# Kernel optimization log

Hardware: AMD Instinct MI355X
Metric: run time of the kernel (lower is better)

Reference implementation:

```python
import jax, jax.numpy as jnp
import numpy as np

N_E, FEAT, REST = 2048, 512, 8
HEAD, LENGTH = 8, 64


def setup_inputs() -> dict:
    key = jax.random.key(0)
    kx, kq, kk, kd = jax.random.split(key, 4)
    x = jax.random.normal(kx, (N_E, FEAT, REST), dtype=jnp.float32)
    Q = jax.random.normal(kq, (HEAD, LENGTH, FEAT), dtype=jnp.float32)
    K = jax.random.normal(kk, (HEAD, LENGTH, FEAT), dtype=jnp.float32)
    D = jax.random.normal(kd, (HEAD, LENGTH, FEAT), dtype=jnp.float32)
    return {"x": x, "Q": Q, "K": K, "D": D}


def _linear(a, W):
    # a: (n, f, *rest), W: (h, q, f) -> y: (n, h, q, *rest)
    y = jnp.einsum('nf...,hqf->nhq...', a, W)
    # L2-normalize over the last 3 axes (here: h? no -- axes (q, rest...) per the
    # original code: sum over (-1,-2,-3) of (n,h,q,rest) = (h,q,rest) per n)
    norm = jnp.sqrt((y * y).sum((-1, -2, -3), keepdims=True))
    return y / norm


def reference(x, Q, K, D):
    n_e = x.shape[0]
    rest = x.shape[2:]
    head, length = Q.shape[0], Q.shape[1]
    q = _linear(x, Q)  # (n, h, l, rest)
    k = _linear(x, K)
    d = _linear(x, D)
    # scores over electrons: contract (l, rest) -> (h, n, n)
    w = jax.nn.softmax(jnp.einsum('nh...,mh...->hnm', q, k), axis=-1)
    # weighted combine: (h,n,m) x (m,h,l,rest) -> (n,h,l,rest)
    v = jnp.einsum('hnm,mhl...->nhl...', w, d)
    return v.reshape((n_e, head * length) + rest)
```

## Files before the change

### kernel.cpp

```cpp
#include <hip/hip_runtime.h>
#include <math.h>

#define NE   2048
#define FEAT 512

typedef short short8 __attribute__((ext_vector_type(8)));
typedef float f32x4  __attribute__((ext_vector_type(4)));

__device__ __forceinline__ unsigned short f2bf(float f) {
    union { float f; unsigned u; } v; v.f = f;
    unsigned r = v.u + 0x7fffu + ((v.u >> 16) & 1u);
    return (unsigned short)(r >> 16);
}
__device__ __forceinline__ float bf2f(unsigned b) {
    union { unsigned u; float f; } v; v.u = b << 16;
    return v.f;
}
__device__ __forceinline__ unsigned pack2(float a, float b) {
    return (unsigned)f2bf(a) | ((unsigned)f2bf(b) << 16);
}

__device__ __forceinline__ void gld16(unsigned short* lds, const unsigned short* g) {
    __builtin_amdgcn_global_load_lds(
        (const __attribute__((address_space(1))) unsigned int*)g,
        (__attribute__((address_space(3))) unsigned int*)lds,
        16, 0, 0);
}

__device__ __forceinline__ void bar() {
    asm volatile("" ::: "memory");
    __builtin_amdgcn_s_barrier();
    asm volatile("" ::: "memory");
}
#define VMW(n) asm volatile("s_waitcnt vmcnt(" #n ")" ::: "memory")


__global__ __launch_bounds__(256) void wconv_kernel(
    const float* __restrict__ Wq, const float* __restrict__ Wk, const float* __restrict__ Wd,
    unsigned short* __restrict__ wbf)
{
    const int t = threadIdx.x;
    const float* W = (blockIdx.y == 0) ? Wq : (blockIdx.y == 1) ? Wk : Wd;
    unsigned short* o = wbf + (size_t)blockIdx.y * 262144;
    const int idx = blockIdx.x * 2048 + t * 8;
    const float4* p = (const float4*)(W + idx);
    float4 v0 = p[0], v1 = p[1];
    *(uint4*)(o + idx) = make_uint4(pack2(v0.x, v0.y), pack2(v0.z, v0.w),
                                    pack2(v1.x, v1.y), pack2(v1.z, v1.w));
}

__global__ __launch_bounds__(256) void xpose_kernel(const float* __restrict__ x,
                                                    unsigned short* __restrict__ xt)
{
    __shared__ float xs[8 * 516];
    const int t = threadIdx.x;
    const int n = blockIdx.x;
    const float4* xp = (const float4*)(x + (size_t)n * 4096);
    #pragma unroll
    for (int i = 0; i < 4; ++i) {
        int idx = t + 256 * i;
        float4 v = xp[idx];
        int f = idx >> 1, rh = (idx & 1) * 4;
        xs[(rh + 0) * 516 + f] = v.x;
        xs[(rh + 1) * 516 + f] = v.y;
        xs[(rh + 2) * 516 + f] = v.z;
        xs[(rh + 3) * 516 + f] = v.w;
    }
    __syncthreads();
    const int r = t >> 5, f0 = (t & 31) * 16;
    const float* src = &xs[r * 516 + f0];
    unsigned o[8];
    #pragma unroll
    for (int j = 0; j < 8; ++j) o[j] = pack2(src[2 * j], src[2 * j + 1]);
    unsigned short* dst = xt + (size_t)n * 4096 + r * 512 + f0;
    *(uint4*)dst       = make_uint4(o[0], o[1], o[2], o[3]);
    *(uint4*)(dst + 8) = make_uint4(o[4], o[5], o[6], o[7]);
}

__global__ __launch_bounds__(512, 1) void proj_gemm(
    const unsigned short* __restrict__ wbf, const unsigned short* __restrict__ xt,
    unsigned short* __restrict__ qb, unsigned short* __restrict__ kb, unsigned short* __restrict__ db,
    float* __restrict__ s2)
{
    __shared__ unsigned short SM[49152];
    const int t = threadIdx.x;
    int bid = blockIdx.x + 128 * (blockIdx.y + 2 * blockIdx.z);
    int swz = (bid & 7) * 96 + (bid >> 3);
    const int bx = swz & 127, rest = swz >> 7;
    const int my = rest & 1, w = rest >> 1;
    const unsigned short* W = wbf + (size_t)w * 262144;
    unsigned short* out = (w == 0) ? qb : (w == 1) ? kb : db;
    const int M0 = my * 256;
    const int N0 = bx * 128;
    const int wave = t >> 6, lane = t & 63, quad = lane >> 4, l16 = lane & 15;
    const int wr = wave >> 1, wc = wave & 1;
    const int lrow = lane >> 3;
    const int scol = ((lane & 7) ^ lrow) * 8;

    f32x4 acc[4][4];
    #pragma unroll
    for (int m = 0; m < 4; ++m)
        #pragma unroll
        for (int n = 0; n < 4; ++n) acc[m][n] = {0.f, 0.f, 0.f, 0.f};

    auto STAGE = [&](int kc, int buf) {
        unsigned short* A = SM + buf * 16384;
        unsigned short* B = SM + 32768 + buf * 8192;
        #pragma unroll
        for (int p = 0; p < 4; ++p) {
            int c = p * 8 + wave;
            gld16(A + c * 512, W + (size_t)(M0 + c * 8 + lrow) * 512 + kc * 64 + scol);
        }
        #pragma unroll
        for (int p = 0; p < 2; ++p) {
            int c = p * 8 + wave;
            gld16(B + c * 512, xt + (size_t)(N0 + c * 8 + lrow) * 512 + kc * 64 + scol);
        }
    };
    auto COMPUTE = [&](int buf) {
        const unsigned short* A = SM + buf * 16384;
        const unsigned short* B = SM + 32768 + buf * 8192;
        #pragma unroll
        for (int kk = 0; kk < 2; ++kk) {
            int so = ((kk * 4 + quad) ^ (l16 & 7)) * 8;
            short8 a[4], b[4];
            #pragma unroll
            for (int m = 0; m < 4; ++m)
                a[m] = *(const short8*)&A[(wr * 64 + m * 16 + l16) * 64 + so];
            #pragma unroll
            for (int n = 0; n < 4; ++n)
                b[n] = *(const short8*)&B[(wc * 64 + n * 16 + l16) * 64 + so];
            #pragma unroll
            for (int m = 0; m < 4; ++m)
                #pragma unroll
                for (int n = 0; n < 4; ++n)
                    acc[m][n] = __builtin_amdgcn_mfma_f32_16x16x32_bf16(a[m], b[n], acc[m][n], 0, 0, 0);
        }
    };

    STAGE(0, 0);
    STAGE(1, 1);
    for (int kc = 0; kc < 8; ++kc) {
        if (kc < 7) { VMW(6); } else { VMW(0); }
        bar();
        COMPUTE(kc & 1);
        bar();
        if (kc + 2 < 8) STAGE(kc + 2, kc & 1);
    }

    float cs[4];
    #pragma unroll
    for (int n = 0; n < 4; ++n) {
        float s = 0.f;
        #pragma unroll
        for (int m = 0; m < 4; ++m)
            #pragma unroll
            for (int reg = 0; reg < 4; ++reg)
                s += acc[m][n][reg] * acc[m][n][reg];
        cs[n] = s;
    }
    #pragma unroll
    for (int n = 0; n < 4; ++n) {
        float s = cs[n];
        s += __shfl_xor(s, 16);
        s += __shfl_xor(s, 32);
        s += __shfl_xor(s, 1);
        s += __shfl_xor(s, 2);
        s += __shfl_xor(s, 4);
        if ((lane & 7) == 0 && lane < 16) {
            int n_elec = (N0 >> 3) + wc * 8 + n * 2 + (lane >> 3);
            atomicAdd(&s2[w * NE + n_elec], s);
        }
    }

    unsigned short* T = SM;
    #pragma unroll
    for (int m = 0; m < 4; ++m)
        #pragma unroll
        for (int reg = 0; reg < 4; ++reg) {
            int row = wr * 64 + m * 16 + quad * 4 + reg;
            #pragma unroll
            for (int n = 0; n < 4; ++n)
                T[row * 136 + wc * 64 + n * 16 + l16] = f2bf(acc[m][n][reg]);
        }
    __syncthreads();
    #pragma unroll
    for (int i = 0; i < 8; ++i) {
        int c = t + 512 * i;
        int row = c & 255, cb = c >> 8;
        uint4 v = *(const uint4*)(T + row * 136 + cb * 8);
        int hl = M0 + row;
        unsigned short* dst = out + (size_t)(hl >> 6) * 1048576 + (size_t)(hl & 63) * 8
                                  + (size_t)((N0 >> 3) + cb) * 512;
        *(uint4*)dst = v;
    }
}

__global__ __launch_bounds__(256) void dtrans_kernel(
    const unsigned short* __restrict__ db, const float* __restrict__ s2d,
    unsigned short* __restrict__ dT)
{
    __shared__ float Ts[64 * 68];
    const int t = threadIdx.x;
    const int h = blockIdx.z, n0 = blockIdx.y * 64, f0 = blockIdx.x * 64;
    const int rr = t >> 3, cs = (t & 7) * 8;
    #pragma unroll
    for (int p = 0; p < 2; ++p) {
        int row = rr + p * 32;
        float sc = rsqrtf(s2d[n0 + row]);
        uint4 v = *(const uint4*)(db + ((size_t)h * NE + n0 + row) * 512 + f0 + cs);
        unsigned a[4] = {v.x, v.y, v.z, v.w};
        float* d = &Ts[row * 68 + cs];
        #pragma unroll
        for (int j = 0; j < 4; ++j) {
            d[2 * j]     = bf2f(a[j] & 0xffffu) * sc;
            d[2 * j + 1] = bf2f(a[j] >> 16) * sc;
        }
    }
    __syncthreads();
    const int f = t >> 2, ns = (t & 3) * 16;
    unsigned o[8];
    #pragma unroll
    for (int j = 0; j < 8; ++j)
        o[j] = pack2(Ts[(ns + 2 * j) * 68 + f], Ts[(ns + 2 * j + 1) * 68 + f]);
    unsigned short* dst = dT + ((size_t)h * 512 + f0 + f) * NE + n0 + ns;
    *(uint4*)dst       = make_uint4(o[0], o[1], o[2], o[3]);
    *(uint4*)(dst + 8) = make_uint4(o[4], o[5], o[6], o[7]);
}

__global__ __launch_bounds__(512, 1) void score_kernel(
    const unsigned short* __restrict__ qb, const unsigned short* __restrict__ kb,
    const float* __restrict__ s2, unsigned short* __restrict__ P,
    float* __restrict__ sums, int g)
{
    __shared__ unsigned short SM[49152];
    const int t = threadIdx.x;
    int bid = blockIdx.x + 16 * (blockIdx.y + 8 * blockIdx.z);
    int swz = (bid & 7) * 64 + (bid >> 3);
    const int bx = swz & 15, by = (swz >> 4) & 7, bz = swz >> 7;
    const int hg = bz, h = g * 4 + hg;
    const int n0 = by * 256, m0 = bx * 128;
    const int wave = t >> 6, lane = t & 63, quad = lane >> 4, l16 = lane & 15;
    const int wr = wave >> 1, wc = wave & 1;
    const int lrow = lane >> 3;
    const int scol = ((lane & 7) ^ lrow) * 8;
    const unsigned short* qh = qb + (size_t)h * NE * 512;
    const unsigned short* kh = kb + (size_t)h * NE * 512;

    f32x4 acc[4][4];
    #pragma unroll
    for (int m = 0; m < 4; ++m)
        #pragma unroll
        for (int n = 0; n < 4; ++n) acc[m][n] = {0.f, 0.f, 0.f, 0.f};

    auto STAGE = [&](int kc, int buf) {
        unsigned short* A = SM + buf * 16384;
        unsigned short* B = SM + 32768 + buf * 8192;
        #pragma unroll
        for (int p = 0; p < 4; ++p) {
            int c = p * 8 + wave;
            gld16(A + c * 512, qh + (size_t)(n0 + c * 8 + lrow) * 512 + kc * 64 + scol);
        }
        #pragma unroll
        for (int p = 0; p < 2; ++p) {
            int c = p * 8 + wave;
            gld16(B + c * 512, kh + (size_t)(m0 + c * 8 + lrow) * 512 + kc * 64 + scol);
        }
    };
    auto COMPUTE = [&](int buf) {
        const unsigned short* A = SM + buf * 16384;
        const unsigned short* B = SM + 32768 + buf * 8192;
        #pragma unroll
        for (int kk = 0; kk < 2; ++kk) {
            int so = ((kk * 4 + quad) ^ (l16 & 7)) * 8;
            short8 a[4], b[4];
            #pragma unroll
            for (int m = 0; m < 4; ++m)
                a[m] = *(const short8*)&A[(wr * 64 + m * 16 + l16) * 64 + so];
            #pragma unroll
            for (int n = 0; n < 4; ++n)
                b[n] = *(const short8*)&B[(wc * 64 + n * 16 + l16) * 64 + so];
            #pragma unroll
            for (int m = 0; m < 4; ++m)
                #pragma unroll
                for (int n = 0; n < 4; ++n)
                    acc[m][n] = __builtin_amdgcn_mfma_f32_16x16x32_bf16(a[m], b[n], acc[m][n], 0, 0, 0);
        }
    };

    STAGE(0, 0);
    STAGE(1, 1);
    for (int kc = 0; kc < 8; ++kc) {
        if (kc < 7) { VMW(6); } else { VMW(0); }
        bar();
        COMPUTE(kc & 1);
        bar();
        if (kc + 2 < 8) STAGE(kc + 2, kc & 1);
    }

    float ik[4];
    #pragma unroll
    for (int n = 0; n < 4; ++n) ik[n] = rsqrtf(s2[NE + m0 + wc * 64 + n * 16 + l16]);

    unsigned short* T = SM;
    #pragma unroll
    for (int m = 0; m < 4; ++m)
        #pragma unroll
        for (int reg = 0; reg < 4; ++reg) {
            int row = wr * 64 + m * 16 + quad * 4 + reg;
            float qs = rsqrtf(s2[n0 + row]);
            float rs = 0.f;
            #pragma unroll
            for (int n = 0; n < 4; ++n) {
                float e = __expf(acc[m][n][reg] * qs * ik[n]);
                unsigned short bx16 = f2bf(e);
                T[row * 136 + wc * 64 + n * 16 + l16] = bx16;
                rs += bf2f(bx16);
            }
            rs += __shfl_xor(rs, 1);
            rs += __shfl_xor(rs, 2);
            rs += __shfl_xor(rs, 4);
            rs += __shfl_xor(rs, 8);
            if (l16 == 0) atomicAdd(&sums[hg * NE + n0 + row], rs);
        }
    __syncthreads();
    unsigned short* Ph = P + (size_t)hg * NE * NE;
    #pragma unroll
    for (int i = 0; i < 8; ++i) {
        int c = t + 512 * i;
        int row = c >> 4, cb = c & 15;
        uint4 v = *(const uint4*)(T + row * 136 + cb * 8);
        *(uint4*)(Ph + (size_t)(n0 + row) * NE + m0 + cb * 8) = v;
    }
}

__global__ __launch_bounds__(512, 1) void combine_kernel(
    const unsigned short* __restrict__ P, const unsigned short* __restrict__ dT,
    const float* __restrict__ sums, float* __restrict__ out, int g)
{
    __shared__ unsigned short Ps[2][16384];
    __shared__ unsigned short Ds[2][16384];
    const int t = threadIdx.x;
    int bid = blockIdx.x + 4 * (blockIdx.y + 16 * blockIdx.z);
    int swz = (bid & 7) * 32 + (bid >> 3);
    const int bx = swz & 3, by = (swz >> 2) & 15, bz = swz >> 6;
    const int hg = bz, h = g * 4 + hg;
    const int n0 = by * 128, f0 = bx * 128;
    const int wave = t >> 6, lane = t & 63, quad = lane >> 4, l16 = lane & 15;
    const int wn = wave >> 1, wf = wave & 1;
    const int lrow4 = lane >> 4;
    const unsigned short* Ph = P + (size_t)hg * NE * NE;
    const unsigned short* dh = dT + (size_t)h * 512 * NE;

    f32x4 acc[2][4];
    #pragma unroll
    for (int i = 0; i < 2; ++i)
        #pragma unroll
        for (int j = 0; j < 4; ++j) acc[i][j] = {0.f, 0.f, 0.f, 0.f};

    auto STAGE = [&](int mc, int buf) {
        #pragma unroll
        for (int p = 0; p < 4; ++p) {
            int c = p * 8 + wave;
            int row = c * 4 + lrow4;
            int sb = ((lane & 15) ^ (row & 15)) * 8;
            gld16(&Ps[buf][c * 512], Ph + (size_t)(n0 + row) * NE + mc * 128 + sb);
        }
        #pragma unroll
        for (int p = 0; p < 4; ++p) {
            int c = p * 8 + wave;
            int row = c * 4 + lrow4;
            int sb = ((lane & 15) ^ (row & 15)) * 8;
            gld16(&Ds[buf][c * 512], dh + (size_t)(f0 + row) * NE + mc * 128 + sb);
        }
    };
    auto COMPUTE = [&](int buf) {
        #pragma unroll
        for (int kk = 0; kk < 4; ++kk) {
            int so = ((kk * 4 + quad) ^ l16) * 8;
            short8 a0 = *(const short8*)&Ps[buf][(wn * 32 + l16) * 128 + so];
            short8 a1 = *(const short8*)&Ps[buf][(wn * 32 + 16 + l16) * 128 + so];
            #pragma unroll
            for (int ct = 0; ct < 4; ++ct) {
                short8 bb = *(const short8*)&Ds[buf][(wf * 64 + ct * 16 + l16) * 128 + so];
                acc[0][ct] = __builtin_amdgcn_mfma_f32_16x16x32_bf16(a0, bb, acc[0][ct], 0, 0, 0);
                acc[1][ct] = __builtin_amdgcn_mfma_f32_16x16x32_bf16(a1, bb, acc[1][ct], 0, 0, 0);
            }
        }
    };

    STAGE(0, 0);
    STAGE(1, 1);
    for (int mc = 0; mc < 16; ++mc) {
        if (mc < 15) { VMW(8); } else { VMW(0); }
        bar();
        COMPUTE(mc & 1);
        bar();
        if (mc + 2 < 16) STAGE(mc + 2, mc & 1);
    }

    #pragma unroll
    for (int rt = 0; rt < 2; ++rt)
        #pragma unroll
        for (int reg = 0; reg < 4; ++reg) {
            int nl = wn * 32 + rt * 16 + quad * 4 + reg;
            float li = 1.0f / sums[hg * NE + n0 + nl];
            float* orow = out + (size_t)(n0 + nl) * 4096 + h * 512 + f0 + wf * 64;
            #pragma unroll
            for (int ct = 0; ct < 4; ++ct)
                orow[ct * 16 + l16] = acc[rt][ct][reg] * li;
        }
}

extern "C" void kernel_launch(void* const* d_in, const int* in_sizes, int n_in,
                              void* d_out, int out_size, void* d_ws, size_t ws_size,
                              hipStream_t stream)
{
    const float* x  = (const float*)d_in[0];
    const float* Qw = (const float*)d_in[1];
    const float* Kw = (const float*)d_in[2];
    const float* Dw = (const float*)d_in[3];
    float* out = (float*)d_out;

    char* ws = (char*)d_ws;
    unsigned short* xt = (unsigned short*)ws;
    unsigned short* db = (unsigned short*)(ws + 16777216);
    unsigned short* P  = (unsigned short*)ws;
    unsigned short* qb = (unsigned short*)(ws + 33554432);
    unsigned short* kb = (unsigned short*)(ws + 33554432 + 16777216);
    unsigned short* dT = (unsigned short*)(ws + 33554432 + 2 * 16777216);
    unsigned short* wbf = dT;
    float* sums   = (float*)(ws + 83886080);
    float* s2     = (float*)(ws + 83886080 + 32768);

    wconv_kernel<<<dim3(128, 3), 256, 0, stream>>>(Qw, Kw, Dw, wbf);
    xpose_kernel<<<2048, 256, 0, stream>>>(x, xt);
    hipMemsetAsync(s2, 0, 3 * NE * sizeof(float), stream);
    proj_gemm<<<dim3(128, 2, 3), 512, 0, stream>>>(wbf, xt, qb, kb, db, s2);
    dtrans_kernel<<<dim3(8, 32, 8), 256, 0, stream>>>(db, s2 + 2 * NE, dT);
    for (int g = 0; g < 2; ++g) {
        hipMemsetAsync(sums, 0, 4 * NE * sizeof(float), stream);
        score_kernel<<<dim3(16, 8, 4), 512, 0, stream>>>(qb, kb, s2, P, sums, g);
        combine_kernel<<<dim3(4, 16, 4), 512, 0, stream>>>(P, dT, sums, out, g);
    }
}
```

Measured before the change: 268.4 us.

## Fuse prep kernels, merge memsets, single-buffer score kernel for two blocks per CU

```diff
diff --git a/kernel.cpp b/kernel.cpp
--- a/kernel.cpp
+++ b/kernel.cpp
@@ -35,46 +35,47 @@
 #define VMW(n) asm volatile("s_waitcnt vmcnt(" #n ")" ::: "memory")
 
 
-__global__ __launch_bounds__(256) void wconv_kernel(
+__global__ __launch_bounds__(256) void prep_kernel(
+    const float* __restrict__ x,
     const float* __restrict__ Wq, const float* __restrict__ Wk, const float* __restrict__ Wd,
-    unsigned short* __restrict__ wbf)
-{
-    const int t = threadIdx.x;
-    const float* W = (blockIdx.y == 0) ? Wq : (blockIdx.y == 1) ? Wk : Wd;
-    unsigned short* o = wbf + (size_t)blockIdx.y * 262144;
-    const int idx = blockIdx.x * 2048 + t * 8;
-    const float4* p = (const float4*)(W + idx);
-    float4 v0 = p[0], v1 = p[1];
-    *(uint4*)(o + idx) = make_uint4(pack2(v0.x, v0.y), pack2(v0.z, v0.w),
-                                    pack2(v1.x, v1.y), pack2(v1.z, v1.w));
-}
-
-__global__ __launch_bounds__(256) void xpose_kernel(const float* __restrict__ x,
-                                                    unsigned short* __restrict__ xt)
+    unsigned short* __restrict__ xt, unsigned short* __restrict__ wbf)
 {
     __shared__ float xs[8 * 516];
     const int t = threadIdx.x;
-    const int n = blockIdx.x;
-    const float4* xp = (const float4*)(x + (size_t)n * 4096);
-    #pragma unroll
-    for (int i = 0; i < 4; ++i) {
-        int idx = t + 256 * i;
-        float4 v = xp[idx];
-        int f = idx >> 1, rh = (idx & 1) * 4;
-        xs[(rh + 0) * 516 + f] = v.x;
-        xs[(rh + 1) * 516 + f] = v.y;
-        xs[(rh + 2) * 516 + f] = v.z;
-        xs[(rh + 3) * 516 + f] = v.w;
-    }
-    __syncthreads();
-    const int r = t >> 5, f0 = (t & 31) * 16;
-    const float* src = &xs[r * 516 + f0];
-    unsigned o[8];
-    #pragma unroll
-    for (int j = 0; j < 8; ++j) o[j] = pack2(src[2 * j], src[2 * j + 1]);
-    unsigned short* dst = xt + (size_t)n * 4096 + r * 512 + f0;
-    *(uint4*)dst       = make_uint4(o[0], o[1], o[2], o[3]);
-    *(uint4*)(dst + 8) = make_uint4(o[4], o[5], o[6], o[7]);
+    const int bid = blockIdx.x;
+    if (bid < 2048) {
+        const int n = bid;
+        const float4* xp = (const float4*)(x + (size_t)n * 4096);
+        #pragma unroll
+        for (int i = 0; i < 4; ++i) {
+            int idx = t + 256 * i;
+            float4 v = xp[idx];
+            int f = idx >> 1, rh = (idx & 1) * 4;
+            xs[(rh + 0) * 516 + f] = v.x;
+            xs[(rh + 1) * 516 + f] = v.y;
+            xs[(rh + 2) * 516 + f] = v.z;
+            xs[(rh + 3) * 516 + f] = v.w;
+        }
+        __syncthreads();
+        const int r = t >> 5, f0 = (t & 31) * 16;
+        const float* src = &xs[r * 516 + f0];
+        unsigned o[8];
+        #pragma unroll
+        for (int j = 0; j < 8; ++j) o[j] = pack2(src[2 * j], src[2 * j + 1]);
+        unsigned short* dst = xt + (size_t)n * 4096 + r * 512 + f0;
+        *(uint4*)dst       = make_uint4(o[0], o[1], o[2], o[3]);
+        *(uint4*)(dst + 8) = make_uint4(o[4], o[5], o[6], o[7]);
+    } else {
+        const int b = bid - 2048;
+        const int wy = b >> 7, wx = b & 127;
+        const float* W = (wy == 0) ? Wq : (wy == 1) ? Wk : Wd;
+        unsigned short* o = wbf + (size_t)wy * 262144;
+        const int idx = wx * 2048 + t * 8;
+        const float4* p = (const float4*)(W + idx);
+        float4 v0 = p[0], v1 = p[1];
+        *(uint4*)(o + idx) = make_uint4(pack2(v0.x, v0.y), pack2(v0.z, v0.w),
+                                        pack2(v1.x, v1.y), pack2(v1.z, v1.w));
+    }
 }
 
 __global__ __launch_bounds__(512, 1) void proj_gemm(
@@ -228,12 +229,12 @@
     *(uint4*)(dst + 8) = make_uint4(o[4], o[5], o[6], o[7]);
 }
 
-__global__ __launch_bounds__(512, 1) void score_kernel(
+__global__ __launch_bounds__(512, 2) void score_kernel(
     const unsigned short* __restrict__ qb, const unsigned short* __restrict__ kb,
     const float* __restrict__ s2, unsigned short* __restrict__ P,
     float* __restrict__ sums, int g)
 {
-    __shared__ unsigned short SM[49152];
+    __shared__ unsigned short SM[34816];
     const int t = threadIdx.x;
     int bid = blockIdx.x + 16 * (blockIdx.y + 8 * blockIdx.z);
     int swz = (bid & 7) * 64 + (bid >> 3);
@@ -246,6 +247,8 @@
     const int scol = ((lane & 7) ^ lrow) * 8;
     const unsigned short* qh = qb + (size_t)h * NE * 512;
     const unsigned short* kh = kb + (size_t)h * NE * 512;
+    unsigned short* A = SM;
+    unsigned short* B = SM + 16384;
 
     f32x4 acc[4][4];
     #pragma unroll
@@ -253,9 +256,7 @@
         #pragma unroll
         for (int n = 0; n < 4; ++n) acc[m][n] = {0.f, 0.f, 0.f, 0.f};
 
-    auto STAGE = [&](int kc, int buf) {
-        unsigned short* A = SM + buf * 16384;
-        unsigned short* B = SM + 32768 + buf * 8192;
+    for (int kc = 0; kc < 8; ++kc) {
         #pragma unroll
         for (int p = 0; p < 4; ++p) {
             int c = p * 8 + wave;
@@ -266,10 +267,7 @@
             int c = p * 8 + wave;
             gld16(B + c * 512, kh + (size_t)(m0 + c * 8 + lrow) * 512 + kc * 64 + scol);
         }
-    };
-    auto COMPUTE = [&](int buf) {
-        const unsigned short* A = SM + buf * 16384;
-        const unsigned short* B = SM + 32768 + buf * 8192;
+        __syncthreads();
         #pragma unroll
         for (int kk = 0; kk < 2; ++kk) {
             int so = ((kk * 4 + quad) ^ (l16 & 7)) * 8;
@@ -286,16 +284,7 @@
                 for (int n = 0; n < 4; ++n)
                     acc[m][n] = __builtin_amdgcn_mfma_f32_16x16x32_bf16(a[m], b[n], acc[m][n], 0, 0, 0);
         }
-    };
-
-    STAGE(0, 0);
-    STAGE(1, 1);
-    for (int kc = 0; kc < 8; ++kc) {
-        if (kc < 7) { VMW(6); } else { VMW(0); }
-        bar();
-        COMPUTE(kc & 1);
-        bar();
-        if (kc + 2 < 8) STAGE(kc + 2, kc & 1);
+        __syncthreads();
     }
 
     float ik[4];
@@ -431,16 +420,15 @@
     unsigned short* dT = (unsigned short*)(ws + 33554432 + 2 * 16777216);
     unsigned short* wbf = dT;
     float* sums   = (float*)(ws + 83886080);
-    float* s2     = (float*)(ws + 83886080 + 32768);
-
-    wconv_kernel<<<dim3(128, 3), 256, 0, stream>>>(Qw, Kw, Dw, wbf);
-    xpose_kernel<<<2048, 256, 0, stream>>>(x, xt);
-    hipMemsetAsync(s2, 0, 3 * NE * sizeof(float), stream);
+    float* s2     = (float*)(ws + 83886080 + 65536);
+
+    hipMemsetAsync(sums, 0, 65536 + 24576, stream);
+    prep_kernel<<<2432, 256, 0, stream>>>(x, Qw, Kw, Dw, xt, wbf);
     proj_gemm<<<dim3(128, 2, 3), 512, 0, stream>>>(wbf, xt, qb, kb, db, s2);
     dtrans_kernel<<<dim3(8, 32, 8), 256, 0, stream>>>(db, s2 + 2 * NE, dT);
     for (int g = 0; g < 2; ++g) {
-        hipMemsetAsync(sums, 0, 4 * NE * sizeof(float), stream);
-        score_kernel<<<dim3(16, 8, 4), 512, 0, stream>>>(qb, kb, s2, P, sums, g);
-        combine_kernel<<<dim3(4, 16, 4), 512, 0, stream>>>(P, dT, sums, out, g);
-    }
-}
+        float* sums_g = sums + g * 4 * NE;
+        score_kernel<<<dim3(16, 8, 4), 512, 0, stream>>>(qb, kb, s2, P, sums_g, g);
+        combine_kernel<<<dim3(4, 16, 4), 512, 0, stream>>>(P, dT, sums_g, out, g);
+    }
+}
```

Measured after the change: 239.9 us. 1.12x faster.
